# Kernel optimization log

Measured on AMD Instinct MI355X. Metric: run time of the kernel, lower is better.

## Reference

```python
import jax, jax.numpy as jnp
import numpy as np

VDIM, HDIM, B = 128, 512, 512
EPS = 1e-5  # torch LayerNorm default


def _ln(x, g, b):
    m = x.mean(-1, keepdims=True)
    v = ((x - m) ** 2).mean(-1, keepdims=True)
    return (x - m) * jax.lax.rsqrt(v + EPS) * g + b


def setup_inputs() -> dict:
    key = jax.random.key(0)
    ks = jax.random.split(key, 16)
    s = 0.05  # small init so sigmoids/logs stay numerically tame
    d = {}
    d["u"] = jax.random.uniform(ks[0], (VDIM, B), jnp.float32)
    d["q_w1"] = s * jax.random.normal(ks[1], (VDIM, HDIM), jnp.float32)
    d["q_b1"] = jnp.zeros((HDIM,), jnp.float32)
    d["q_g1"] = jnp.ones((HDIM,), jnp.float32)
    d["q_be1"] = jnp.zeros((HDIM,), jnp.float32)
    d["q_w2"] = s * jax.random.normal(ks[2], (HDIM, HDIM), jnp.float32)
    d["q_b2"] = jnp.zeros((HDIM,), jnp.float32)
    d["q_g2"] = jnp.ones((HDIM,), jnp.float32)
    d["q_be2"] = jnp.zeros((HDIM,), jnp.float32)
    d["q_w3"] = s * jax.random.normal(ks[3], (HDIM, HDIM), jnp.float32)
    d["q_b3"] = jnp.zeros((HDIM,), jnp.float32)
    d["q_g3"] = jnp.ones((HDIM,), jnp.float32)
    d["q_be3"] = jnp.zeros((HDIM,), jnp.float32)
    d["q_W"] = 0.01 * jax.random.normal(ks[4], (VDIM, HDIM), jnp.float32)  # per-node output heads
    d["q_bias"] = jnp.zeros((VDIM,), jnp.float32)
    d["q_marg"] = jnp.zeros((VDIM,), jnp.float32)
    d["f_w1"] = s * jax.random.normal(ks[5], (VDIM, HDIM), jnp.float32)
    d["f_b1"] = jnp.zeros((HDIM,), jnp.float32)
    d["f_g1"] = jnp.ones((HDIM,), jnp.float32)
    d["f_be1"] = jnp.zeros((HDIM,), jnp.float32)
    d["f_w2"] = s * jax.random.normal(ks[6], (HDIM, HDIM), jnp.float32)
    d["f_b2"] = jnp.zeros((HDIM,), jnp.float32)
    d["f_g2"] = jnp.ones((HDIM,), jnp.float32)
    d["f_be2"] = jnp.zeros((HDIM,), jnp.float32)
    d["f_w3"] = s * jax.random.normal(ks[7], (HDIM, HDIM), jnp.float32)
    d["f_b3"] = jnp.zeros((HDIM,), jnp.float32)
    d["f_g3"] = jnp.ones((HDIM,), jnp.float32)
    d["f_be3"] = jnp.zeros((HDIM,), jnp.float32)
    d["f_w4"] = s * jax.random.normal(ks[8], (HDIM,), jnp.float32)
    d["f_b4"] = jnp.zeros((1,), jnp.float32)
    d["J"] = 0.1 * jax.random.normal(ks[9], (VDIM, VDIM), jnp.float32)  # Ising couplings for scorer
    d["top_order"] = jnp.arange(VDIM, dtype=jnp.int32)
    d["pa_mask"] = jax.random.randint(ks[10], (VDIM, VDIM), 0, 2, jnp.int32)
    return d


def reference(u, q_w1, q_b1, q_g1, q_be1, q_w2, q_b2, q_g2, q_be2,
              q_w3, q_b3, q_g3, q_be3, q_W, q_bias, q_marg,
              f_w1, f_b1, f_g1, f_be1, f_w2, f_b2, f_g2, f_be2,
              f_w3, f_b3, f_g3, f_be3, f_w4, f_b4, J,
              top_order, pa_mask):
    def qtrunk(V):
        h = jax.nn.relu(_ln(V @ q_w1 + q_b1, q_g1, q_be1))
        h = jax.nn.relu(_ln(h @ q_w2 + q_b2, q_g2, q_be2))
        h = jax.nn.relu(_ln(h @ q_w3 + q_b3, q_g3, q_be3))
        return h  # [B, H]

    def fnet(V):
        h = jax.nn.relu(_ln(V @ f_w1 + f_b1, f_g1, f_be1))
        h = jax.nn.relu(_ln(h @ f_w2 + f_b2, f_g2, f_be2))
        h = jax.nn.relu(_ln(h @ f_w3 + f_b3, f_g3, f_be3))
        return h @ f_w4 + f_b4[0]  # [B]

    # gather per-node quantities in topological order once, outside the scan
    masks = pa_mask[top_order].astype(u.dtype)          # [V, V] parent masks
    Wq = q_W[top_order]                                  # [V, H]
    bq = q_bias[top_order]                               # [V]
    mg = q_marg[top_order]                               # [V]
    oh = jax.nn.one_hot(top_order, VDIM, dtype=u.dtype)  # [V, V]

    def step(V, xs):
        mask_i, Wq_i, bq_i, mg_i, oh_i, u_i = xs
        V_pa = V * mask_i                                # [B, V] parents only
        x = qtrunk(V_pa) @ Wq_i + bq_i                   # [B]
        empty = jnp.abs(V_pa).sum(1) == 0
        p_on = jnp.where(empty, jax.nn.sigmoid(mg_i), jax.nn.sigmoid(x))
        samp = u_i < p_on                                # bernoulli(p_on)
        v_samp = 2.0 * samp.astype(u.dtype) - 1.0
        V_new = V * (1.0 - oh_i) + v_samp[:, None] * oh_i  # scatter into column
        lp = jnp.where(samp, jnp.log(p_on), jnp.log1p(-p_on))
        logF = fnet(jax.lax.stop_gradient(V_new))        # V.clone().detach()
        return V_new, (lp, logF)

    V0 = jnp.zeros((B, VDIM), u.dtype)
    V, (lps, logFs) = jax.lax.scan(step, V0, (masks, Wq, bq, mg, oh, u))
    log_pf = lps.T                                       # [B, V]
    F0 = fnet(V0)                                        # log_flow[:, 0] (alg='db')
    score = jax.lax.stop_gradient(jnp.einsum('bi,ij,bj->b', V, J, V))  # -energy, detached
    # last logF is overwritten by the terminal score, as in the original
    log_flow = jnp.concatenate([F0[:, None], logFs[:-1].T, score[:, None]], axis=1)  # [B, V+1]
    loss = ((log_flow[:, :-1] + log_pf - log_flow[:, 1:]) ** 2).mean(1).mean()
    return V, loss
```

## Files before the change

### kernel.cpp

```cpp
#include <hip/hip_runtime.h>
#include <hip/hip_bf16.h>
#include <math.h>

#define VDIM 128
#define HDIM 512
#define BATCH 512
#define RPB 4
#define NBLK (BATCH / RPB)
#define NWORK 128
#define NT 512
#define NWAVE 8
#define LN_EPS 1e-5f
#define FROWS 32
#define NGRP 16
#define SBPG 8

__device__ __forceinline__ float4 f4zero() { return make_float4(0.f, 0.f, 0.f, 0.f); }
__device__ __forceinline__ float4 f4add(float4 a, float4 b) {
    return make_float4(a.x + b.x, a.y + b.y, a.z + b.z, a.w + b.w);
}
__device__ __forceinline__ float4 f4fma(float4 a, float s, float4 c) {
    return make_float4(fmaf(a.x, s, c.x), fmaf(a.y, s, c.y),
                       fmaf(a.z, s, c.z), fmaf(a.w, s, c.w));
}
__device__ __forceinline__ float4 f4scale(float4 a, float s) {
    return make_float4(a.x * s, a.y * s, a.z * s, a.w * s);
}
__device__ __forceinline__ float4 f4sub(float4 a, float4 b) {
    return make_float4(a.x - b.x, a.y - b.y, a.z - b.z, a.w - b.w);
}
__device__ __forceinline__ float f4get(float4 v, int r) {
    return r == 0 ? v.x : r == 1 ? v.y : r == 2 ? v.z : v.w;
}

struct Params {
    const float *u;
    const float *q_w1, *q_b1, *q_g1, *q_be1;
    const float *q_w2, *q_b2, *q_g2, *q_be2;
    const float *q_w3, *q_b3, *q_g3, *q_be3;
    const float *q_W, *q_bias, *q_marg;
    const float *f_w1, *f_b1, *f_g1, *f_be1;
    const float *f_w2, *f_b2, *f_g2, *f_be2;
    const float *f_w3, *f_b3, *f_g3, *f_be3;
    const float *f_w4, *f_b4, *J;
    const int *top_order, *pa_mask;
    int *wflag;
    float *V_out, *lp, *lf, *score, *vs, *loss;
};

struct ScanS {
    float4 VT[VDIM];
    float4 VPT[VDIM];
    float4 ATa[HDIM];
    float4 ATb[HDIM];
    float4 part[4][4][128];
    float4 red2[NWAVE][2];
    float4 redH[NWAVE];
    int ord[VDIM];
    int emptyb[VDIM];
};
struct WorkS {
    float Vt[VDIM * FROWS];
    float A[HDIM * FROWS];
    int ord[VDIM], invp[VDIM];
    float4 redA[NWAVE], redB[NWAVE];
};
union SMem { ScanS s; WorkS w; };

__device__ __forceinline__ float4 allreduce4_1s(float4 v, float4 *red, int tid) {
#pragma unroll
    for (int off = 1; off < 64; off <<= 1) {
        v.x += __shfl_xor(v.x, off, 64);
        v.y += __shfl_xor(v.y, off, 64);
        v.z += __shfl_xor(v.z, off, 64);
        v.w += __shfl_xor(v.w, off, 64);
    }
    if ((tid & 63) == 0) red[tid >> 6] = v;
    __syncthreads();
    float4 s = red[0];
#pragma unroll
    for (int w = 1; w < NWAVE; ++w) s = f4add(s, red[w]);
    return s;
}

__device__ __forceinline__ void allreduce2_1s(float4 &a, float4 &b,
                                              float4 (*red)[2], int tid) {
#pragma unroll
    for (int off = 1; off < 64; off <<= 1) {
        a.x += __shfl_xor(a.x, off, 64); a.y += __shfl_xor(a.y, off, 64);
        a.z += __shfl_xor(a.z, off, 64); a.w += __shfl_xor(a.w, off, 64);
        b.x += __shfl_xor(b.x, off, 64); b.y += __shfl_xor(b.y, off, 64);
        b.z += __shfl_xor(b.z, off, 64); b.w += __shfl_xor(b.w, off, 64);
    }
    if ((tid & 63) == 0) { red[tid >> 6][0] = a; red[tid >> 6][1] = b; }
    __syncthreads();
    float4 sa = red[0][0], sb = red[0][1];
#pragma unroll
    for (int w = 1; w < NWAVE; ++w) { sa = f4add(sa, red[w][0]); sb = f4add(sb, red[w][1]); }
    a = sa; b = sb;
}

__device__ __forceinline__ float block_reduce1(float v, float *red, int tid) {
#pragma unroll
    for (int off = 1; off < 64; off <<= 1) v += __shfl_xor(v, off, 64);
    if ((tid & 63) == 0) red[tid >> 6] = v;
    __syncthreads();
    float s = 0.f;
#pragma unroll
    for (int w = 0; w < NWAVE; ++w) s += red[w];
    __syncthreads();
    return s;
}

__device__ __forceinline__ void redpair(float4 &a, float4 &b,
                                        float4 *redA, float4 *redB, int tid) {
#pragma unroll
    for (int off = 1; off < 64; off <<= 1) {
        a.x += __shfl_xor(a.x, off, 64); a.y += __shfl_xor(a.y, off, 64);
        a.z += __shfl_xor(a.z, off, 64); a.w += __shfl_xor(a.w, off, 64);
        b.x += __shfl_xor(b.x, off, 64); b.y += __shfl_xor(b.y, off, 64);
        b.z += __shfl_xor(b.z, off, 64); b.w += __shfl_xor(b.w, off, 64);
    }
    int w = tid >> 6;
    if ((tid & 63) == 0) { redA[w] = a; redB[w] = b; }
    __syncthreads();
    int p = w ^ 1;
    a = f4add(redA[w], redA[p]);
    b = f4add(redB[w], redB[p]);
    __syncthreads();
}

template <int K>
__device__ __forceinline__ void gemv_ln_scan(const float4 *__restrict__ inA,
                                             const float *__restrict__ W,
                                             const float *__restrict__ bias,
                                             const float *__restrict__ gam,
                                             const float *__restrict__ bet,
                                             float4 *__restrict__ outA,
                                             ScanS &S, int tid, int ks, int cq,
                                             int myc) {
    constexpr int kc = K / 4;
    constexpr int q4 = kc / 4;
    constexpr int seg = K / 4;
    const float4 *Wp = (const float4 *)W + (size_t)(ks * kc) * (HDIM / 4) + cq;
    const float4 *ap = inA + ks * q4;
    float4 acc0 = f4zero(), acc1 = f4zero(), acc2 = f4zero(), acc3 = f4zero();
#pragma unroll 4
    for (int q = 0; q < q4; ++q) {
        float4 a0 = ap[q];
        float4 a1 = ap[q + seg];
        float4 a2 = ap[q + 2 * seg];
        float4 a3 = ap[q + 3 * seg];
        float4 w0 = Wp[(size_t)(4 * q + 0) * (HDIM / 4)];
        float4 w1 = Wp[(size_t)(4 * q + 1) * (HDIM / 4)];
        float4 w2 = Wp[(size_t)(4 * q + 2) * (HDIM / 4)];
        float4 w3 = Wp[(size_t)(4 * q + 3) * (HDIM / 4)];
        acc0 = f4fma(a0, w0.x, acc0); acc1 = f4fma(a0, w0.y, acc1);
        acc2 = f4fma(a0, w0.z, acc2); acc3 = f4fma(a0, w0.w, acc3);
        acc0 = f4fma(a1, w1.x, acc0); acc1 = f4fma(a1, w1.y, acc1);
        acc2 = f4fma(a1, w1.z, acc2); acc3 = f4fma(a1, w1.w, acc3);
        acc0 = f4fma(a2, w2.x, acc0); acc1 = f4fma(a2, w2.y, acc1);
        acc2 = f4fma(a2, w2.z, acc2); acc3 = f4fma(a2, w2.w, acc3);
        acc0 = f4fma(a3, w3.x, acc0); acc1 = f4fma(a3, w3.y, acc1);
        acc2 = f4fma(a3, w3.z, acc2); acc3 = f4fma(a3, w3.w, acc3);
    }
    S.part[0][ks][cq] = acc0;
    S.part[1][ks][cq] = acc1;
    S.part[2][ks][cq] = acc2;
    S.part[3][ks][cq] = acc3;
    __syncthreads();
    const int j = ks, cb = cq;
    float4 z = f4add(f4add(S.part[j][0][cb], S.part[j][1][cb]),
                     f4add(S.part[j][2][cb], S.part[j][3][cb]));
    float bc = bias[myc];
    z.x += bc; z.y += bc; z.z += bc; z.w += bc;
    const float inv = 1.f / (float)HDIM;
    float4 s1 = z;
    float4 s2 = make_float4(z.x * z.x, z.y * z.y, z.z * z.z, z.w * z.w);
    allreduce2_1s(s1, s2, S.red2, tid);
    float4 m = f4scale(s1, inv);
    float4 e2 = f4scale(s2, inv);
    float4 var = make_float4(fmaxf(e2.x - m.x * m.x, 0.f),
                             fmaxf(e2.y - m.y * m.y, 0.f),
                             fmaxf(e2.z - m.z * m.z, 0.f),
                             fmaxf(e2.w - m.w * m.w, 0.f));
    float4 rs;
    rs.x = 1.f / sqrtf(var.x + LN_EPS);
    rs.y = 1.f / sqrtf(var.y + LN_EPS);
    rs.z = 1.f / sqrtf(var.z + LN_EPS);
    rs.w = 1.f / sqrtf(var.w + LN_EPS);
    float4 d = f4sub(z, m);
    float gc = gam[myc], ec = bet[myc];
    float4 h;
    h.x = fmaxf(fmaf(d.x * rs.x, gc, ec), 0.f);
    h.y = fmaxf(fmaf(d.y * rs.y, gc, ec), 0.f);
    h.z = fmaxf(fmaf(d.z * rs.z, gc, ec), 0.f);
    h.w = fmaxf(fmaf(d.w * rs.w, gc, ec), 0.f);
    outA[tid] = h;
    __syncthreads();
}

__device__ void scan_role(const Params &P, int bid, ScanS &S) {
    const int tid = threadIdx.x;
    const int ks = tid >> 7;
    const int cq = tid & 127;
    const int myc = 4 * cq + ks;
    const int row0 = bid * RPB;

    if (tid < VDIM) { S.VT[tid] = f4zero(); S.ord[tid] = P.top_order[tid]; }
    __syncthreads();
    if (tid < VDIM) {
        int nd = S.ord[tid];
        int mm = 0;
        for (int jj = 0; jj < tid; ++jj) mm |= P.pa_mask[nd * VDIM + S.ord[jj]];
        S.emptyb[tid] = (mm == 0);
        S.VPT[(tid & 3) * 32 + (tid >> 2)] = f4zero();
    }
    __syncthreads();

    for (int i = 0; i < VDIM; ++i) {
        const int node = S.ord[i];

        gemv_ln_scan<VDIM>(S.VPT, P.q_w1, P.q_b1, P.q_g1, P.q_be1, S.ATa, S, tid, ks, cq, myc);
        gemv_ln_scan<HDIM>(S.ATa, P.q_w2, P.q_b2, P.q_g2, P.q_be2, S.ATb, S, tid, ks, cq, myc);
        gemv_ln_scan<HDIM>(S.ATb, P.q_w3, P.q_b3, P.q_g3, P.q_be3, S.ATa, S, tid, ks, cq, myc);

        float wq = P.q_W[(size_t)node * HDIM + myc];
        float4 x4 = allreduce4_1s(f4scale(S.ATa[tid], wq), S.redH, tid);

        {
            const bool empty = (S.emptyb[i] != 0);
            const float qb = P.q_bias[node];
            const float mg = P.q_marg[node];
            float a0 = empty ? mg : x4.x + qb;
            float a1 = empty ? mg : x4.y + qb;
            float a2 = empty ? mg : x4.z + qb;
            float a3 = empty ? mg : x4.w + qb;
            float4 pv = make_float4(1.f / (1.f + expf(-a0)), 1.f / (1.f + expf(-a1)),
                                    1.f / (1.f + expf(-a2)), 1.f / (1.f + expf(-a3)));
            float4 uv = *(const float4 *)(P.u + (size_t)i * BATCH + row0);
            float4 newv = make_float4(uv.x < pv.x ? 1.f : -1.f,
                                      uv.y < pv.y ? 1.f : -1.f,
                                      uv.z < pv.z ? 1.f : -1.f,
                                      uv.w < pv.w ? 1.f : -1.f);
            if (tid < VDIM) {
                float mk = 0.f;
                if (i + 1 < VDIM) {
                    int nodeN = S.ord[i + 1];
                    mk = (float)P.pa_mask[nodeN * VDIM + tid];
                }
                float4 vk = S.VT[tid];
                if (tid == node) { vk = newv; S.VT[tid] = newv; }
                S.VPT[(tid & 3) * 32 + (tid >> 2)] = f4scale(vk, mk);
            }
            if (tid < RPB) {
                float pr = f4get(pv, tid);
                float vr = f4get(newv, tid);
                __hip_atomic_store(&P.vs[(size_t)i * BATCH + row0 + tid], vr,
                                   __ATOMIC_RELAXED, __HIP_MEMORY_SCOPE_AGENT);
                P.lp[(size_t)i * BATCH + row0 + tid] =
                    (vr > 0.f) ? logf(pr) : log1pf(-pr);
            }
            __syncthreads();
            if (tid == 0)
                __hip_atomic_store(P.wflag + bid, i + 1,
                                   __ATOMIC_RELEASE, __HIP_MEMORY_SCOPE_AGENT);
        }
    }

    float4 inner = f4zero();
    if (tid < VDIM) {
#pragma unroll 4
        for (int ii = 0; ii < VDIM; ++ii)
            inner = f4fma(S.VT[ii], P.J[(size_t)ii * VDIM + tid], inner);
        float4 vc = S.VT[tid];
        inner = make_float4(inner.x * vc.x, inner.y * vc.y, inner.z * vc.z, inner.w * vc.w);
    }
    float4 sc4 = allreduce4_1s(inner, S.redH, tid);
    if (tid < RPB) P.score[row0 + tid] = f4get(sc4, tid);
    if (tid < VDIM) {
        float4 v = S.VT[tid];
        P.V_out[(size_t)(row0 + 0) * VDIM + tid] = v.x;
        P.V_out[(size_t)(row0 + 1) * VDIM + tid] = v.y;
        P.V_out[(size_t)(row0 + 2) * VDIM + tid] = v.z;
        P.V_out[(size_t)(row0 + 3) * VDIM + tid] = v.w;
    }
}

template <int K>
__device__ __forceinline__ void flayer512(const float *__restrict__ in,
                                          const float *__restrict__ W,
                                          const float *__restrict__ bias,
                                          const float *__restrict__ gam,
                                          const float *__restrict__ bet,
                                          float *__restrict__ out,
                                          float4 *redA, float4 *redB, int tid) {
    const int rh = tid >> 7;
    const int cq = tid & 127;
    const float4 *Wv = (const float4 *)W + cq;
    float4 accA[4], accB[4];
#pragma unroll
    for (int j = 0; j < 4; ++j) { accA[j] = f4zero(); accB[j] = f4zero(); }
#pragma unroll 4
    for (int k = 0; k < K; ++k) {
        float4 w = Wv[(size_t)k * (HDIM / 4)];
        const float *ip = in + k * FROWS + 8 * rh;
        float4 vA = *(const float4 *)ip;
        float4 vB = *(const float4 *)(ip + 4);
        accA[0] = f4fma(vA, w.x, accA[0]); accB[0] = f4fma(vB, w.x, accB[0]);
        accA[1] = f4fma(vA, w.y, accA[1]); accB[1] = f4fma(vB, w.y, accB[1]);
        accA[2] = f4fma(vA, w.z, accA[2]); accB[2] = f4fma(vB, w.z, accB[2]);
        accA[3] = f4fma(vA, w.w, accA[3]); accB[3] = f4fma(vB, w.w, accB[3]);
    }
    float4 b4 = ((const float4 *)bias)[cq];
    float bb[4] = {b4.x, b4.y, b4.z, b4.w};
#pragma unroll
    for (int j = 0; j < 4; ++j) {
        accA[j].x += bb[j]; accA[j].y += bb[j]; accA[j].z += bb[j]; accA[j].w += bb[j];
        accB[j].x += bb[j]; accB[j].y += bb[j]; accB[j].z += bb[j]; accB[j].w += bb[j];
    }
    const float inv = 1.f / (float)HDIM;
    float4 sA = f4add(f4add(accA[0], accA[1]), f4add(accA[2], accA[3]));
    float4 sB = f4add(f4add(accB[0], accB[1]), f4add(accB[2], accB[3]));
    redpair(sA, sB, redA, redB, tid);
    float4 mA = f4scale(sA, inv), mB = f4scale(sB, inv);
    float4 dA[4], dB[4];
    float4 qA = f4zero(), qB = f4zero();
#pragma unroll
    for (int j = 0; j < 4; ++j) {
        dA[j] = f4sub(accA[j], mA);
        dB[j] = f4sub(accB[j], mB);
        qA.x += dA[j].x * dA[j].x; qA.y += dA[j].y * dA[j].y;
        qA.z += dA[j].z * dA[j].z; qA.w += dA[j].w * dA[j].w;
        qB.x += dB[j].x * dB[j].x; qB.y += dB[j].y * dB[j].y;
        qB.z += dB[j].z * dB[j].z; qB.w += dB[j].w * dB[j].w;
    }
    redpair(qA, qB, redA, redB, tid);
    float4 rsA, rsB;
    rsA.x = 1.f / sqrtf(qA.x * inv + LN_EPS); rsA.y = 1.f / sqrtf(qA.y * inv + LN_EPS);
    rsA.z = 1.f / sqrtf(qA.z * inv + LN_EPS); rsA.w = 1.f / sqrtf(qA.w * inv + LN_EPS);
    rsB.x = 1.f / sqrtf(qB.x * inv + LN_EPS); rsB.y = 1.f / sqrtf(qB.y * inv + LN_EPS);
    rsB.z = 1.f / sqrtf(qB.z * inv + LN_EPS); rsB.w = 1.f / sqrtf(qB.w * inv + LN_EPS);
    float4 g4 = ((const float4 *)gam)[cq];
    float4 e4 = ((const float4 *)bet)[cq];
    float gg[4] = {g4.x, g4.y, g4.z, g4.w};
    float ee[4] = {e4.x, e4.y, e4.z, e4.w};
#pragma unroll
    for (int j = 0; j < 4; ++j) {
        float4 hA, hB;
        hA.x = fmaxf(fmaf(dA[j].x * rsA.x, gg[j], ee[j]), 0.f);
        hA.y = fmaxf(fmaf(dA[j].y * rsA.y, gg[j], ee[j]), 0.f);
        hA.z = fmaxf(fmaf(dA[j].z * rsA.z, gg[j], ee[j]), 0.f);
        hA.w = fmaxf(fmaf(dA[j].w * rsA.w, gg[j], ee[j]), 0.f);
        hB.x = fmaxf(fmaf(dB[j].x * rsB.x, gg[j], ee[j]), 0.f);
        hB.y = fmaxf(fmaf(dB[j].y * rsB.y, gg[j], ee[j]), 0.f);
        hB.z = fmaxf(fmaf(dB[j].z * rsB.z, gg[j], ee[j]), 0.f);
        hB.w = fmaxf(fmaf(dB[j].w * rsB.w, gg[j], ee[j]), 0.f);
        float *op = out + (4 * cq + j) * FROWS + 8 * rh;
        *(float4 *)op = hA;
        *(float4 *)(op + 4) = hB;
    }
    __syncthreads();
}

__device__ void worker_role(const Params &P, int wid, WorkS &S) {
    const int tid = threadIdx.x;
    if (tid < VDIM) S.ord[tid] = P.top_order[tid];
    __syncthreads();
    if (tid < VDIM) S.invp[S.ord[tid]] = tid;
    __syncthreads();
    const int g = wid & (NGRP - 1);
    const int r0 = g * FROWS;

    for (int tile = wid; tile < VDIM * NGRP; tile += NWORK) {
        const int t = tile >> 4;
        if (t == VDIM - 1) continue;
        if (tid < SBPG) {
            const int need = t + 1;
            while (__hip_atomic_load(P.wflag + (SBPG * g + tid),
                                     __ATOMIC_RELAXED,
                                     __HIP_MEMORY_SCOPE_AGENT) < need)
                __builtin_amdgcn_s_sleep(4);
        }
        __syncthreads();
        for (int idx = tid; idx < VDIM * FROWS; idx += NT) {
            int k = idx >> 5, rr = idx & (FROWS - 1);
            int s = S.invp[k];
            S.Vt[idx] = (s <= t)
                ? __hip_atomic_load(&P.vs[(size_t)s * BATCH + r0 + rr],
                                    __ATOMIC_RELAXED, __HIP_MEMORY_SCOPE_AGENT)
                : 0.f;
        }
        __syncthreads();

        flayer512<VDIM>(S.Vt, P.f_w1, P.f_b1, P.f_g1, P.f_be1, S.A, S.redA, S.redB, tid);
        flayer512<HDIM>(S.A, P.f_w2, P.f_b2, P.f_g2, P.f_be2, S.A, S.redA, S.redB, tid);
        flayer512<HDIM>(S.A, P.f_w3, P.f_b3, P.f_g3, P.f_be3, S.A, S.redA, S.redB, tid);

        const int rh = tid >> 7, cq = tid & 127;
        float4 w4 = ((const float4 *)P.f_w4)[cq];
        float ww[4] = {w4.x, w4.y, w4.z, w4.w};
        float4 sA = f4zero(), sB = f4zero();
#pragma unroll
        for (int j = 0; j < 4; ++j) {
            const float *ap2 = S.A + (4 * cq + j) * FROWS + 8 * rh;
            float4 vA = *(const float4 *)ap2;
            float4 vB = *(const float4 *)(ap2 + 4);
            sA = f4fma(vA, ww[j], sA);
            sB = f4fma(vB, ww[j], sB);
        }
        redpair(sA, sB, S.redA, S.redB, tid);
        if (cq == 0) {
            float b4v = P.f_b4[0];
            float *dst = P.lf + (size_t)t * BATCH + r0 + 8 * rh;
            dst[0] = sA.x + b4v; dst[1] = sA.y + b4v;
            dst[2] = sA.z + b4v; dst[3] = sA.w + b4v;
            dst[4] = sB.x + b4v; dst[5] = sB.y + b4v;
            dst[6] = sB.z + b4v; dst[7] = sB.w + b4v;
        }
        __syncthreads();
    }
}

__global__ __launch_bounds__(NT) void gfn_main(Params P) {
    __shared__ SMem sm;
    const int xcd = blockIdx.x & 7;
    const int grp = blockIdx.x >> 3;
    if (xcd < 4) scan_role(P, grp * 4 + xcd, sm.s);
    else         worker_role(P, grp * 4 + (xcd - 4), sm.w);
}

__global__ __launch_bounds__(NT) void gfn_loss(Params P) {
    __shared__ float H1[HDIM], H2[HDIM];
    __shared__ float red1[NWAVE];
    const int tid = threadIdx.x;
    const float inv = 1.f / (float)HDIM;

    float z = P.f_b1[tid];
    float m = block_reduce1(z, red1, tid) * inv;
    float d = z - m;
    float var = block_reduce1(d * d, red1, tid) * inv;
    float h = fmaxf(fmaf(d * (1.f / sqrtf(var + LN_EPS)), P.f_g1[tid], P.f_be1[tid]), 0.f);
    H1[tid] = h;
    __syncthreads();

    float acc = 0.f;
    for (int k = 0; k < HDIM; ++k) acc = fmaf(H1[k], P.f_w2[(size_t)k * HDIM + tid], acc);
    z = acc + P.f_b2[tid];
    m = block_reduce1(z, red1, tid) * inv;
    d = z - m;
    var = block_reduce1(d * d, red1, tid) * inv;
    h = fmaxf(fmaf(d * (1.f / sqrtf(var + LN_EPS)), P.f_g2[tid], P.f_be2[tid]), 0.f);
    H2[tid] = h;
    __syncthreads();

    acc = 0.f;
    for (int k = 0; k < HDIM; ++k) acc = fmaf(H2[k], P.f_w3[(size_t)k * HDIM + tid], acc);
    z = acc + P.f_b3[tid];
    m = block_reduce1(z, red1, tid) * inv;
    d = z - m;
    var = block_reduce1(d * d, red1, tid) * inv;
    h = fmaxf(fmaf(d * (1.f / sqrtf(var + LN_EPS)), P.f_g3[tid], P.f_be3[tid]), 0.f);
    float F0 = block_reduce1(h * P.f_w4[tid], red1, tid) + P.f_b4[0];

    const int b = tid;
    float lfp = F0;
    float s = 0.f;
    for (int t = 0; t < VDIM; ++t) {
        float lp = P.lp[(size_t)t * BATCH + b];
        float lfn = (t == VDIM - 1) ? P.score[b] : P.lf[(size_t)t * BATCH + b];
        float dd = lfp + lp - lfn;
        s = fmaf(dd, dd, s);
        lfp = lfn;
    }
    s *= (1.f / (float)VDIM);
    float total = block_reduce1(s, red1, tid) * (1.f / (float)BATCH);
    if (tid == 0) P.loss[0] = total;
}

extern "C" void kernel_launch(void *const *d_in, const int *in_sizes, int n_in,
                              void *d_out, int out_size, void *d_ws, size_t ws_size,
                              hipStream_t stream) {
    Params P;
    P.u     = (const float *)d_in[0];
    P.q_w1  = (const float *)d_in[1];
    P.q_b1  = (const float *)d_in[2];
    P.q_g1  = (const float *)d_in[3];
    P.q_be1 = (const float *)d_in[4];
    P.q_w2  = (const float *)d_in[5];
    P.q_b2  = (const float *)d_in[6];
    P.q_g2  = (const float *)d_in[7];
    P.q_be2 = (const float *)d_in[8];
    P.q_w3  = (const float *)d_in[9];
    P.q_b3  = (const float *)d_in[10];
    P.q_g3  = (const float *)d_in[11];
    P.q_be3 = (const float *)d_in[12];
    P.q_W   = (const float *)d_in[13];
    P.q_bias= (const float *)d_in[14];
    P.q_marg= (const float *)d_in[15];
    P.f_w1  = (const float *)d_in[16];
    P.f_b1  = (const float *)d_in[17];
    P.f_g1  = (const float *)d_in[18];
    P.f_be1 = (const float *)d_in[19];
    P.f_w2  = (const float *)d_in[20];
    P.f_b2  = (const float *)d_in[21];
    P.f_g2  = (const float *)d_in[22];
    P.f_be2 = (const float *)d_in[23];
    P.f_w3  = (const float *)d_in[24];
    P.f_b3  = (const float *)d_in[25];
    P.f_g3  = (const float *)d_in[26];
    P.f_be3 = (const float *)d_in[27];
    P.f_w4  = (const float *)d_in[28];
    P.f_b4  = (const float *)d_in[29];
    P.J     = (const float *)d_in[30];
    P.top_order = (const int *)d_in[31];
    P.pa_mask   = (const int *)d_in[32];

    float *ws = (float *)d_ws;
    P.V_out = (float *)d_out;
    P.loss  = (float *)d_out + (size_t)BATCH * VDIM;
    P.lp    = ws;
    P.lf    = ws + (size_t)VDIM * BATCH;
    P.score = ws + 2 * (size_t)VDIM * BATCH;
    P.vs    = ws + 2 * (size_t)VDIM * BATCH + BATCH;
    P.wflag = (int *)(ws + 3 * (size_t)VDIM * BATCH + BATCH);

    hipMemsetAsync(P.wflag, 0, NBLK * sizeof(int), stream);
    gfn_main<<<dim3(NBLK + NWORK), dim3(NT), 0, stream>>>(P);
    gfn_loss<<<dim3(1), dim3(NT), 0, stream>>>(P);
}
```

Before: 3.843 ms.

## Process eight batch rows per scan block with 8-way K split

Each scan block now handles 8 batch rows instead of 4, so every weight element loaded from memory is reused across twice as many rows, and the number of scan blocks drops from 128 to 64. The GEMV is restructured with an 8-way K split, lo/hi row halves and a permuted activation layout, and the LayerNorm reductions are batched into one 4-vector allreduce. The third layer keeps its output in registers instead of writing it to shared memory. The trade-off is more accumulator registers per thread, less block-level parallelism in the serial scan, and an extra sync round for the two-phase partial-sum reduction.

```diff
diff --git a/kernel.cpp b/kernel.cpp
--- a/kernel.cpp
+++ b/kernel.cpp
@@ -5,15 +5,16 @@
 #define VDIM 128
 #define HDIM 512
 #define BATCH 512
-#define RPB 4
-#define NBLK (BATCH / RPB)
+#define RPB 8
+#define NSCAN 64
 #define NWORK 128
 #define NT 512
 #define NWAVE 8
+#define KSPL 8
 #define LN_EPS 1e-5f
 #define FROWS 32
 #define NGRP 16
-#define SBPG 8
+#define SPG 4
 
 __device__ __forceinline__ float4 f4zero() { return make_float4(0.f, 0.f, 0.f, 0.f); }
 __device__ __forceinline__ float4 f4add(float4 a, float4 b) {
@@ -28,6 +29,9 @@
 }
 __device__ __forceinline__ float4 f4sub(float4 a, float4 b) {
     return make_float4(a.x - b.x, a.y - b.y, a.z - b.z, a.w - b.w);
+}
+__device__ __forceinline__ float4 f4sq(float4 a) {
+    return make_float4(a.x * a.x, a.y * a.y, a.z * a.z, a.w * a.w);
 }
 __device__ __forceinline__ float f4get(float4 v, int r) {
     return r == 0 ? v.x : r == 1 ? v.y : r == 2 ? v.z : v.w;
@@ -49,13 +53,13 @@
 };
 
 struct ScanS {
-    float4 VT[VDIM];
-    float4 VPT[VDIM];
-    float4 ATa[HDIM];
-    float4 ATb[HDIM];
-    float4 part[4][4][128];
-    float4 red2[NWAVE][2];
-    float4 redH[NWAVE];
+    float4 VT[VDIM][2];
+    float4 VPTlo[VDIM], VPThi[VDIM];
+    float4 Alo[HDIM], Ahi[HDIM];
+    float4 Blo[HDIM], Bhi[HDIM];
+    float4 part[4][KSPL][128];
+    float4 red4x[NWAVE][4];
+    float4 red2x[NWAVE][2];
     int ord[VDIM];
     int emptyb[VDIM];
 };
@@ -67,20 +71,8 @@
 };
 union SMem { ScanS s; WorkS w; };
 
-__device__ __forceinline__ float4 allreduce4_1s(float4 v, float4 *red, int tid) {
-#pragma unroll
-    for (int off = 1; off < 64; off <<= 1) {
-        v.x += __shfl_xor(v.x, off, 64);
-        v.y += __shfl_xor(v.y, off, 64);
-        v.z += __shfl_xor(v.z, off, 64);
-        v.w += __shfl_xor(v.w, off, 64);
-    }
-    if ((tid & 63) == 0) red[tid >> 6] = v;
-    __syncthreads();
-    float4 s = red[0];
-#pragma unroll
-    for (int w = 1; w < NWAVE; ++w) s = f4add(s, red[w]);
-    return s;
+__device__ __forceinline__ int stpos(int c) {
+    return 256 * (c >> 8) + 64 * (c & 3) + ((c & 255) >> 2);
 }
 
 __device__ __forceinline__ void allreduce2_1s(float4 &a, float4 &b,
@@ -100,26 +92,52 @@
     a = sa; b = sb;
 }
 
-__device__ __forceinline__ float block_reduce1(float v, float *red, int tid) {
-#pragma unroll
-    for (int off = 1; off < 64; off <<= 1) v += __shfl_xor(v, off, 64);
-    if ((tid & 63) == 0) red[tid >> 6] = v;
-    __syncthreads();
-    float s = 0.f;
-#pragma unroll
-    for (int w = 0; w < NWAVE; ++w) s += red[w];
-    __syncthreads();
-    return s;
-}
-
-__device__ __forceinline__ void redpair(float4 &a, float4 &b,
-                                        float4 *redA, float4 *redB, int tid) {
+__device__ __forceinline__ void allreduce4_1s(float4 &a, float4 &b,
+                                              float4 &c, float4 &d,
+                                              float4 (*red)[4], int tid) {
 #pragma unroll
     for (int off = 1; off < 64; off <<= 1) {
         a.x += __shfl_xor(a.x, off, 64); a.y += __shfl_xor(a.y, off, 64);
         a.z += __shfl_xor(a.z, off, 64); a.w += __shfl_xor(a.w, off, 64);
         b.x += __shfl_xor(b.x, off, 64); b.y += __shfl_xor(b.y, off, 64);
         b.z += __shfl_xor(b.z, off, 64); b.w += __shfl_xor(b.w, off, 64);
+        c.x += __shfl_xor(c.x, off, 64); c.y += __shfl_xor(c.y, off, 64);
+        c.z += __shfl_xor(c.z, off, 64); c.w += __shfl_xor(c.w, off, 64);
+        d.x += __shfl_xor(d.x, off, 64); d.y += __shfl_xor(d.y, off, 64);
+        d.z += __shfl_xor(d.z, off, 64); d.w += __shfl_xor(d.w, off, 64);
+    }
+    int w = tid >> 6;
+    if ((tid & 63) == 0) { red[w][0] = a; red[w][1] = b; red[w][2] = c; red[w][3] = d; }
+    __syncthreads();
+    float4 sa = red[0][0], sb = red[0][1], sc = red[0][2], sd = red[0][3];
+#pragma unroll
+    for (int q = 1; q < NWAVE; ++q) {
+        sa = f4add(sa, red[q][0]); sb = f4add(sb, red[q][1]);
+        sc = f4add(sc, red[q][2]); sd = f4add(sd, red[q][3]);
+    }
+    a = sa; b = sb; c = sc; d = sd;
+}
+
+__device__ __forceinline__ float block_reduce1(float v, float *red, int tid) {
+#pragma unroll
+    for (int off = 1; off < 64; off <<= 1) v += __shfl_xor(v, off, 64);
+    if ((tid & 63) == 0) red[tid >> 6] = v;
+    __syncthreads();
+    float s = 0.f;
+#pragma unroll
+    for (int w = 0; w < NWAVE; ++w) s += red[w];
+    __syncthreads();
+    return s;
+}
+
+__device__ __forceinline__ void redpair(float4 &a, float4 &b,
+                                        float4 *redA, float4 *redB, int tid) {
+#pragma unroll
+    for (int off = 1; off < 64; off <<= 1) {
+        a.x += __shfl_xor(a.x, off, 64); a.y += __shfl_xor(a.y, off, 64);
+        a.z += __shfl_xor(a.z, off, 64); a.w += __shfl_xor(a.w, off, 64);
+        b.x += __shfl_xor(b.x, off, 64); b.y += __shfl_xor(b.y, off, 64);
+        b.z += __shfl_xor(b.z, off, 64); b.w += __shfl_xor(b.w, off, 64);
     }
     int w = tid >> 6;
     if ((tid & 63) == 0) { redA[w] = a; redB[w] = b; }
@@ -130,132 +148,170 @@
     __syncthreads();
 }
 
-template <int K>
-__device__ __forceinline__ void gemv_ln_scan(const float4 *__restrict__ inA,
-                                             const float *__restrict__ W,
-                                             const float *__restrict__ bias,
-                                             const float *__restrict__ gam,
-                                             const float *__restrict__ bet,
-                                             float4 *__restrict__ outA,
-                                             ScanS &S, int tid, int ks, int cq,
-                                             int myc) {
-    constexpr int kc = K / 4;
-    constexpr int q4 = kc / 4;
-    constexpr int seg = K / 4;
-    const float4 *Wp = (const float4 *)W + (size_t)(ks * kc) * (HDIM / 4) + cq;
-    const float4 *ap = inA + ks * q4;
-    float4 acc0 = f4zero(), acc1 = f4zero(), acc2 = f4zero(), acc3 = f4zero();
-#pragma unroll 4
-    for (int q = 0; q < q4; ++q) {
-        float4 a0 = ap[q];
-        float4 a1 = ap[q + seg];
-        float4 a2 = ap[q + 2 * seg];
-        float4 a3 = ap[q + 3 * seg];
-        float4 w0 = Wp[(size_t)(4 * q + 0) * (HDIM / 4)];
-        float4 w1 = Wp[(size_t)(4 * q + 1) * (HDIM / 4)];
-        float4 w2 = Wp[(size_t)(4 * q + 2) * (HDIM / 4)];
-        float4 w3 = Wp[(size_t)(4 * q + 3) * (HDIM / 4)];
-        acc0 = f4fma(a0, w0.x, acc0); acc1 = f4fma(a0, w0.y, acc1);
-        acc2 = f4fma(a0, w0.z, acc2); acc3 = f4fma(a0, w0.w, acc3);
-        acc0 = f4fma(a1, w1.x, acc0); acc1 = f4fma(a1, w1.y, acc1);
-        acc2 = f4fma(a1, w1.z, acc2); acc3 = f4fma(a1, w1.w, acc3);
-        acc0 = f4fma(a2, w2.x, acc0); acc1 = f4fma(a2, w2.y, acc1);
-        acc2 = f4fma(a2, w2.z, acc2); acc3 = f4fma(a2, w2.w, acc3);
-        acc0 = f4fma(a3, w3.x, acc0); acc1 = f4fma(a3, w3.y, acc1);
-        acc2 = f4fma(a3, w3.z, acc2); acc3 = f4fma(a3, w3.w, acc3);
-    }
-    S.part[0][ks][cq] = acc0;
-    S.part[1][ks][cq] = acc1;
-    S.part[2][ks][cq] = acc2;
-    S.part[3][ks][cq] = acc3;
-    __syncthreads();
-    const int j = ks, cb = cq;
-    float4 z = f4add(f4add(S.part[j][0][cb], S.part[j][1][cb]),
-                     f4add(S.part[j][2][cb], S.part[j][3][cb]));
+template <int K, bool LIN, bool WOUT>
+__device__ __forceinline__ void gemv8_ln(const float4 *__restrict__ inLo,
+                                         const float4 *__restrict__ inHi,
+                                         const float *__restrict__ W,
+                                         const float *__restrict__ bias,
+                                         const float *__restrict__ gam,
+                                         const float *__restrict__ bet,
+                                         float4 *__restrict__ outLo,
+                                         float4 *__restrict__ outHi,
+                                         ScanS &S, int tid, int ks, int cq,
+                                         int myc, int myj, int mycb,
+                                         float4 &hLo, float4 &hHi) {
+    constexpr int kc = K / KSPL;
+    const float4 *WA = (const float4 *)W + cq;
+    const float4 *WB = WA + 64;
+    float4 aAl0 = f4zero(), aAl1 = f4zero(), aAl2 = f4zero(), aAl3 = f4zero();
+    float4 aAh0 = f4zero(), aAh1 = f4zero(), aAh2 = f4zero(), aAh3 = f4zero();
+    float4 aBl0 = f4zero(), aBl1 = f4zero(), aBl2 = f4zero(), aBl3 = f4zero();
+    float4 aBh0 = f4zero(), aBh1 = f4zero(), aBh2 = f4zero(), aBh3 = f4zero();
+#pragma unroll 2
+    for (int q = 0; q < kc; ++q) {
+        const int k = ks * kc + q;
+        const int pos = LIN ? k : stpos(k);
+        float4 alo = inLo[pos];
+        float4 ahi = inHi[pos];
+        float4 wa = WA[(size_t)k * (HDIM / 4)];
+        float4 wb = WB[(size_t)k * (HDIM / 4)];
+        aAl0 = f4fma(alo, wa.x, aAl0); aAh0 = f4fma(ahi, wa.x, aAh0);
+        aAl1 = f4fma(alo, wa.y, aAl1); aAh1 = f4fma(ahi, wa.y, aAh1);
+        aAl2 = f4fma(alo, wa.z, aAl2); aAh2 = f4fma(ahi, wa.z, aAh2);
+        aAl3 = f4fma(alo, wa.w, aAl3); aAh3 = f4fma(ahi, wa.w, aAh3);
+        aBl0 = f4fma(alo, wb.x, aBl0); aBh0 = f4fma(ahi, wb.x, aBh0);
+        aBl1 = f4fma(alo, wb.y, aBl1); aBh1 = f4fma(ahi, wb.y, aBh1);
+        aBl2 = f4fma(alo, wb.z, aBl2); aBh2 = f4fma(ahi, wb.z, aBh2);
+        aBl3 = f4fma(alo, wb.w, aBl3); aBh3 = f4fma(ahi, wb.w, aBh3);
+    }
+    S.part[0][ks][cq] = aAl0; S.part[1][ks][cq] = aAl1;
+    S.part[2][ks][cq] = aAl2; S.part[3][ks][cq] = aAl3;
+    S.part[0][ks][64 + cq] = aBl0; S.part[1][ks][64 + cq] = aBl1;
+    S.part[2][ks][64 + cq] = aBl2; S.part[3][ks][64 + cq] = aBl3;
+    __syncthreads();
+    float4 zlo = S.part[myj][0][mycb];
+#pragma unroll
+    for (int s = 1; s < KSPL; ++s) zlo = f4add(zlo, S.part[myj][s][mycb]);
+    __syncthreads();
+    S.part[0][ks][cq] = aAh0; S.part[1][ks][cq] = aAh1;
+    S.part[2][ks][cq] = aAh2; S.part[3][ks][cq] = aAh3;
+    S.part[0][ks][64 + cq] = aBh0; S.part[1][ks][64 + cq] = aBh1;
+    S.part[2][ks][64 + cq] = aBh2; S.part[3][ks][64 + cq] = aBh3;
+    __syncthreads();
+    float4 zhi = S.part[myj][0][mycb];
+#pragma unroll
+    for (int s = 1; s < KSPL; ++s) zhi = f4add(zhi, S.part[myj][s][mycb]);
+
     float bc = bias[myc];
-    z.x += bc; z.y += bc; z.z += bc; z.w += bc;
+    zlo.x += bc; zlo.y += bc; zlo.z += bc; zlo.w += bc;
+    zhi.x += bc; zhi.y += bc; zhi.z += bc; zhi.w += bc;
+
     const float inv = 1.f / (float)HDIM;
-    float4 s1 = z;
-    float4 s2 = make_float4(z.x * z.x, z.y * z.y, z.z * z.z, z.w * z.w);
-    allreduce2_1s(s1, s2, S.red2, tid);
-    float4 m = f4scale(s1, inv);
-    float4 e2 = f4scale(s2, inv);
-    float4 var = make_float4(fmaxf(e2.x - m.x * m.x, 0.f),
-                             fmaxf(e2.y - m.y * m.y, 0.f),
-                             fmaxf(e2.z - m.z * m.z, 0.f),
-                             fmaxf(e2.w - m.w * m.w, 0.f));
-    float4 rs;
-    rs.x = 1.f / sqrtf(var.x + LN_EPS);
-    rs.y = 1.f / sqrtf(var.y + LN_EPS);
-    rs.z = 1.f / sqrtf(var.z + LN_EPS);
-    rs.w = 1.f / sqrtf(var.w + LN_EPS);
-    float4 d = f4sub(z, m);
+    float4 s1l = zlo, s1h = zhi, s2l = f4sq(zlo), s2h = f4sq(zhi);
+    allreduce4_1s(s1l, s1h, s2l, s2h, S.red4x, tid);
+    float4 ml = f4scale(s1l, inv), mh = f4scale(s1h, inv);
+    float4 e2l = f4scale(s2l, inv), e2h = f4scale(s2h, inv);
+    float4 vl = make_float4(fmaxf(e2l.x - ml.x * ml.x, 0.f), fmaxf(e2l.y - ml.y * ml.y, 0.f),
+                            fmaxf(e2l.z - ml.z * ml.z, 0.f), fmaxf(e2l.w - ml.w * ml.w, 0.f));
+    float4 vh = make_float4(fmaxf(e2h.x - mh.x * mh.x, 0.f), fmaxf(e2h.y - mh.y * mh.y, 0.f),
+                            fmaxf(e2h.z - mh.z * mh.z, 0.f), fmaxf(e2h.w - mh.w * mh.w, 0.f));
+    float4 rl, rh;
+    rl.x = 1.f / sqrtf(vl.x + LN_EPS); rl.y = 1.f / sqrtf(vl.y + LN_EPS);
+    rl.z = 1.f / sqrtf(vl.z + LN_EPS); rl.w = 1.f / sqrtf(vl.w + LN_EPS);
+    rh.x = 1.f / sqrtf(vh.x + LN_EPS); rh.y = 1.f / sqrtf(vh.y + LN_EPS);
+    rh.z = 1.f / sqrtf(vh.z + LN_EPS); rh.w = 1.f / sqrtf(vh.w + LN_EPS);
+    float4 dl = f4sub(zlo, ml), dh = f4sub(zhi, mh);
     float gc = gam[myc], ec = bet[myc];
-    float4 h;
-    h.x = fmaxf(fmaf(d.x * rs.x, gc, ec), 0.f);
-    h.y = fmaxf(fmaf(d.y * rs.y, gc, ec), 0.f);
-    h.z = fmaxf(fmaf(d.z * rs.z, gc, ec), 0.f);
-    h.w = fmaxf(fmaf(d.w * rs.w, gc, ec), 0.f);
-    outA[tid] = h;
-    __syncthreads();
+    hLo.x = fmaxf(fmaf(dl.x * rl.x, gc, ec), 0.f);
+    hLo.y = fmaxf(fmaf(dl.y * rl.y, gc, ec), 0.f);
+    hLo.z = fmaxf(fmaf(dl.z * rl.z, gc, ec), 0.f);
+    hLo.w = fmaxf(fmaf(dl.w * rl.w, gc, ec), 0.f);
+    hHi.x = fmaxf(fmaf(dh.x * rh.x, gc, ec), 0.f);
+    hHi.y = fmaxf(fmaf(dh.y * rh.y, gc, ec), 0.f);
+    hHi.z = fmaxf(fmaf(dh.z * rh.z, gc, ec), 0.f);
+    hHi.w = fmaxf(fmaf(dh.w * rh.w, gc, ec), 0.f);
+    if (WOUT) {
+        outLo[tid] = hLo;
+        outHi[tid] = hHi;
+        __syncthreads();
+    }
 }
 
 __device__ void scan_role(const Params &P, int bid, ScanS &S) {
     const int tid = threadIdx.x;
-    const int ks = tid >> 7;
-    const int cq = tid & 127;
-    const int myc = 4 * cq + ks;
+    const int ks = tid >> 6;
+    const int cq = tid & 63;
+    const int myc = 4 * (tid & 63) + ((tid >> 6) & 3) + 256 * (tid >> 8);
+    const int myj = (tid >> 6) & 3;
+    const int mycb = (tid & 63) + 64 * (tid >> 8);
     const int row0 = bid * RPB;
 
-    if (tid < VDIM) { S.VT[tid] = f4zero(); S.ord[tid] = P.top_order[tid]; }
+    if (tid < VDIM) {
+        S.VT[tid][0] = f4zero(); S.VT[tid][1] = f4zero();
+        S.ord[tid] = P.top_order[tid];
+    }
     __syncthreads();
     if (tid < VDIM) {
         int nd = S.ord[tid];
         int mm = 0;
         for (int jj = 0; jj < tid; ++jj) mm |= P.pa_mask[nd * VDIM + S.ord[jj]];
         S.emptyb[tid] = (mm == 0);
-        S.VPT[(tid & 3) * 32 + (tid >> 2)] = f4zero();
-    }
-    __syncthreads();
-
+        S.VPTlo[tid] = f4zero();
+        S.VPThi[tid] = f4zero();
+    }
+    __syncthreads();
+
+    float4 hLo, hHi;
     for (int i = 0; i < VDIM; ++i) {
         const int node = S.ord[i];
 
-        gemv_ln_scan<VDIM>(S.VPT, P.q_w1, P.q_b1, P.q_g1, P.q_be1, S.ATa, S, tid, ks, cq, myc);
-        gemv_ln_scan<HDIM>(S.ATa, P.q_w2, P.q_b2, P.q_g2, P.q_be2, S.ATb, S, tid, ks, cq, myc);
-        gemv_ln_scan<HDIM>(S.ATb, P.q_w3, P.q_b3, P.q_g3, P.q_be3, S.ATa, S, tid, ks, cq, myc);
+        gemv8_ln<VDIM, true, true>(S.VPTlo, S.VPThi, P.q_w1, P.q_b1, P.q_g1, P.q_be1,
+                                   S.Alo, S.Ahi, S, tid, ks, cq, myc, myj, mycb, hLo, hHi);
+        gemv8_ln<HDIM, false, true>(S.Alo, S.Ahi, P.q_w2, P.q_b2, P.q_g2, P.q_be2,
+                                    S.Blo, S.Bhi, S, tid, ks, cq, myc, myj, mycb, hLo, hHi);
+        gemv8_ln<HDIM, false, false>(S.Blo, S.Bhi, P.q_w3, P.q_b3, P.q_g3, P.q_be3,
+                                     nullptr, nullptr, S, tid, ks, cq, myc, myj, mycb, hLo, hHi);
 
         float wq = P.q_W[(size_t)node * HDIM + myc];
-        float4 x4 = allreduce4_1s(f4scale(S.ATa[tid], wq), S.redH, tid);
+        float4 xl = f4scale(hLo, wq), xh = f4scale(hHi, wq);
+        allreduce2_1s(xl, xh, S.red2x, tid);
 
         {
             const bool empty = (S.emptyb[i] != 0);
             const float qb = P.q_bias[node];
             const float mg = P.q_marg[node];
-            float a0 = empty ? mg : x4.x + qb;
-            float a1 = empty ? mg : x4.y + qb;
-            float a2 = empty ? mg : x4.z + qb;
-            float a3 = empty ? mg : x4.w + qb;
-            float4 pv = make_float4(1.f / (1.f + expf(-a0)), 1.f / (1.f + expf(-a1)),
-                                    1.f / (1.f + expf(-a2)), 1.f / (1.f + expf(-a3)));
-            float4 uv = *(const float4 *)(P.u + (size_t)i * BATCH + row0);
-            float4 newv = make_float4(uv.x < pv.x ? 1.f : -1.f,
-                                      uv.y < pv.y ? 1.f : -1.f,
-                                      uv.z < pv.z ? 1.f : -1.f,
-                                      uv.w < pv.w ? 1.f : -1.f);
+            float4 pl, ph;
+            pl.x = 1.f / (1.f + expf(-(empty ? mg : xl.x + qb)));
+            pl.y = 1.f / (1.f + expf(-(empty ? mg : xl.y + qb)));
+            pl.z = 1.f / (1.f + expf(-(empty ? mg : xl.z + qb)));
+            pl.w = 1.f / (1.f + expf(-(empty ? mg : xl.w + qb)));
+            ph.x = 1.f / (1.f + expf(-(empty ? mg : xh.x + qb)));
+            ph.y = 1.f / (1.f + expf(-(empty ? mg : xh.y + qb)));
+            ph.z = 1.f / (1.f + expf(-(empty ? mg : xh.z + qb)));
+            ph.w = 1.f / (1.f + expf(-(empty ? mg : xh.w + qb)));
+            const float4 *up = (const float4 *)(P.u + (size_t)i * BATCH + row0);
+            float4 ul = up[0], uh = up[1];
+            float4 nl = make_float4(ul.x < pl.x ? 1.f : -1.f, ul.y < pl.y ? 1.f : -1.f,
+                                    ul.z < pl.z ? 1.f : -1.f, ul.w < pl.w ? 1.f : -1.f);
+            float4 nh = make_float4(uh.x < ph.x ? 1.f : -1.f, uh.y < ph.y ? 1.f : -1.f,
+                                    uh.z < ph.z ? 1.f : -1.f, uh.w < ph.w ? 1.f : -1.f);
             if (tid < VDIM) {
                 float mk = 0.f;
                 if (i + 1 < VDIM) {
                     int nodeN = S.ord[i + 1];
                     mk = (float)P.pa_mask[nodeN * VDIM + tid];
                 }
-                float4 vk = S.VT[tid];
-                if (tid == node) { vk = newv; S.VT[tid] = newv; }
-                S.VPT[(tid & 3) * 32 + (tid >> 2)] = f4scale(vk, mk);
+                float4 vkl = S.VT[tid][0], vkh = S.VT[tid][1];
+                if (tid == node) {
+                    vkl = nl; vkh = nh;
+                    S.VT[tid][0] = nl; S.VT[tid][1] = nh;
+                }
+                S.VPTlo[tid] = f4scale(vkl, mk);
+                S.VPThi[tid] = f4scale(vkh, mk);
             }
             if (tid < RPB) {
-                float pr = f4get(pv, tid);
-                float vr = f4get(newv, tid);
+                float pr = (tid < 4) ? f4get(pl, tid) : f4get(ph, tid - 4);
+                float vr = (tid < 4) ? f4get(nl, tid) : f4get(nh, tid - 4);
                 __hip_atomic_store(&P.vs[(size_t)i * BATCH + row0 + tid], vr,
                                    __ATOMIC_RELAXED, __HIP_MEMORY_SCOPE_AGENT);
                 P.lp[(size_t)i * BATCH + row0 + tid] =
@@ -268,22 +324,31 @@
         }
     }
 
-    float4 inner = f4zero();
+    float4 il = f4zero(), ih = f4zero();
     if (tid < VDIM) {
 #pragma unroll 4
-        for (int ii = 0; ii < VDIM; ++ii)
-            inner = f4fma(S.VT[ii], P.J[(size_t)ii * VDIM + tid], inner);
-        float4 vc = S.VT[tid];
-        inner = make_float4(inner.x * vc.x, inner.y * vc.y, inner.z * vc.z, inner.w * vc.w);
-    }
-    float4 sc4 = allreduce4_1s(inner, S.redH, tid);
-    if (tid < RPB) P.score[row0 + tid] = f4get(sc4, tid);
+        for (int ii = 0; ii < VDIM; ++ii) {
+            float jv = P.J[(size_t)ii * VDIM + tid];
+            il = f4fma(S.VT[ii][0], jv, il);
+            ih = f4fma(S.VT[ii][1], jv, ih);
+        }
+        float4 vl = S.VT[tid][0], vh = S.VT[tid][1];
+        il = make_float4(il.x * vl.x, il.y * vl.y, il.z * vl.z, il.w * vl.w);
+        ih = make_float4(ih.x * vh.x, ih.y * vh.y, ih.z * vh.z, ih.w * vh.w);
+    }
+    allreduce2_1s(il, ih, S.red2x, tid);
+    if (tid < RPB)
+        P.score[row0 + tid] = (tid < 4) ? f4get(il, tid) : f4get(ih, tid - 4);
     if (tid < VDIM) {
-        float4 v = S.VT[tid];
-        P.V_out[(size_t)(row0 + 0) * VDIM + tid] = v.x;
-        P.V_out[(size_t)(row0 + 1) * VDIM + tid] = v.y;
-        P.V_out[(size_t)(row0 + 2) * VDIM + tid] = v.z;
-        P.V_out[(size_t)(row0 + 3) * VDIM + tid] = v.w;
+        float4 vl = S.VT[tid][0], vh = S.VT[tid][1];
+        P.V_out[(size_t)(row0 + 0) * VDIM + tid] = vl.x;
+        P.V_out[(size_t)(row0 + 1) * VDIM + tid] = vl.y;
+        P.V_out[(size_t)(row0 + 2) * VDIM + tid] = vl.z;
+        P.V_out[(size_t)(row0 + 3) * VDIM + tid] = vl.w;
+        P.V_out[(size_t)(row0 + 4) * VDIM + tid] = vh.x;
+        P.V_out[(size_t)(row0 + 5) * VDIM + tid] = vh.y;
+        P.V_out[(size_t)(row0 + 6) * VDIM + tid] = vh.z;
+        P.V_out[(size_t)(row0 + 7) * VDIM + tid] = vh.w;
     }
 }
 
@@ -375,9 +440,9 @@
     for (int tile = wid; tile < VDIM * NGRP; tile += NWORK) {
         const int t = tile >> 4;
         if (t == VDIM - 1) continue;
-        if (tid < SBPG) {
+        if (tid < SPG) {
             const int need = t + 1;
-            while (__hip_atomic_load(P.wflag + (SBPG * g + tid),
+            while (__hip_atomic_load(P.wflag + (SPG * g + tid),
                                      __ATOMIC_RELAXED,
                                      __HIP_MEMORY_SCOPE_AGENT) < need)
                 __builtin_amdgcn_s_sleep(4);
@@ -426,8 +491,12 @@
     __shared__ SMem sm;
     const int xcd = blockIdx.x & 7;
     const int grp = blockIdx.x >> 3;
-    if (xcd < 4) scan_role(P, grp * 4 + xcd, sm.s);
-    else         worker_role(P, grp * 4 + (xcd - 4), sm.w);
+    if (xcd < 4) {
+        const int sid = grp * 4 + xcd;
+        if (sid < NSCAN) scan_role(P, sid, sm.s);
+    } else {
+        worker_role(P, grp * 4 + (xcd - 4), sm.w);
+    }
 }
 
 __global__ __launch_bounds__(NT) void gfn_loss(Params P) {
@@ -525,7 +594,7 @@
     P.vs    = ws + 2 * (size_t)VDIM * BATCH + BATCH;
     P.wflag = (int *)(ws + 3 * (size_t)VDIM * BATCH + BATCH);
 
-    hipMemsetAsync(P.wflag, 0, NBLK * sizeof(int), stream);
-    gfn_main<<<dim3(NBLK + NWORK), dim3(NT), 0, stream>>>(P);
+    hipMemsetAsync(P.wflag, 0, NSCAN * sizeof(int), stream);
+    gfn_main<<<dim3(256), dim3(NT), 0, stream>>>(P);
     gfn_loss<<<dim3(1), dim3(NT), 0, stream>>>(P);
 }
```

After: 5.963 ms. 1.55x slower.
